# Performance work log

Measured on AMD Instinct MI355X. Metric: run time of the kernel, lower is better.

The kernel has to match this reference:

```python
import jax, jax.numpy as jnp
import numpy as np

N_GROUPS = 4


def setup_inputs() -> dict:
    key = jax.random.key(0)
    ks = jax.random.split(key, 6)
    I, J, B = 512, 512, 4  # query tokens, key tokens, grid batch (B = 1 * n_groups)
    n_dim, out_per_group = 128, 4  # n_heads // n_groups = 16 // 4
    grid_q = jax.random.normal(ks[0], (I, 3), dtype=jnp.float32)
    grid_kv = jax.random.normal(ks[1], (B, J, 3), dtype=jnp.float32)
    W1 = jax.random.normal(ks[2], (3, n_dim), dtype=jnp.float32) * (1.0 / np.sqrt(3))
    b1 = jnp.zeros((n_dim,), dtype=jnp.float32)
    W2 = jax.random.normal(ks[3], (n_dim, n_dim), dtype=jnp.float32) * (1.0 / np.sqrt(n_dim))
    b2 = jnp.zeros((n_dim,), dtype=jnp.float32)
    W3 = jax.random.normal(ks[4], (n_dim, out_per_group), dtype=jnp.float32) * (1.0 / np.sqrt(n_dim))
    b3 = jnp.zeros((out_per_group,), dtype=jnp.float32)
    return {"grid_q": grid_q, "grid_kv": grid_kv, "W1": W1, "b1": b1,
            "W2": W2, "b2": b2, "W3": W3, "b3": b3}


def reference(grid_q, grid_kv, W1, b1, W2, b2, W3, b3):
    # grid_q: [I, 3] -> [1, I, 3]; grid_kv: [B, J, 3]
    gq = grid_q[None, :, :]
    # pairwise position difference: [B, I, J, 3]
    pos = gq[:, :, None, :] - grid_kv[:, None, :, :]
    # sign-log transform
    bias = jnp.sign(pos) * jnp.log1p(jnp.abs(pos))
    # tiny MLP: 3 -> n_dim -> n_dim -> heads//groups, pointwise over (B, I, J)
    h = jax.nn.relu(jnp.einsum('bijc,cd->bijd', bias, W1) + b1)
    h = jax.nn.relu(jnp.einsum('bijd,de->bije', h, W2) + b2)
    out = jnp.einsum('bije,eo->bijo', h, W3) + b3  # [B, I, J, O]
    # rearrange '(b g) i j o -> b (g o) i j' with g = N_GROUPS
    B, I, J, O = out.shape
    out = out.reshape(B // N_GROUPS, N_GROUPS, I, J, O)
    out = jnp.transpose(out, (0, 1, 4, 2, 3)).reshape(B // N_GROUPS, N_GROUPS * O, I, J)
    return out
```

## Files before the change

kernel.cpp:

```cpp
#include <hip/hip_runtime.h>
#include <math.h>

#define NBLOCKS 2048
#define THREADS 512
#define TILE 64
#define POS_PER_BLOCK 512
#define ITERS 8
#define CH 512

typedef __attribute__((ext_vector_type(8)))  short  short8;
typedef __attribute__((ext_vector_type(4)))  float  float4v;
typedef __attribute__((ext_vector_type(4)))  unsigned uint4v;
typedef __attribute__((ext_vector_type(16))) float  float16;

__device__ __forceinline__ unsigned cvt_pk(float lo, float hi) {
    unsigned r;
    asm("v_cvt_pk_bf16_f32 %0, %1, %2" : "=v"(r) : "v"(lo), "v"(hi));
    return r;
}


__device__ __forceinline__ int kmap(int c, int jj) {
    return 32 * (c >> 2) + 16 * ((c >> 1) & 1) + 4 * (c & 1) + ((jj >> 2) << 3) + (jj & 3);
}

__global__ __launch_bounds__(512, 4)
void crpb_mfma8(const float* __restrict__ gq,
                const float* __restrict__ gkv,
                const float* __restrict__ W1,
                const float* __restrict__ b1,
                const float* __restrict__ W2,
                const float* __restrict__ b2,
                const float* __restrict__ W3,
                const float* __restrict__ b3,
                float* __restrict__ out)
{
    __shared__ __align__(16) unsigned short ash[2][16 * CH];
    __shared__ __align__(16) float red[2][4 * 4 * 64];
    __shared__ __align__(16) float b2s[128];
    __shared__ __align__(16) unsigned fA[512][4];
    __shared__ __align__(16) unsigned fB[512];

    const int tid  = threadIdx.x;
    const int lane = tid & 63;
    const int w    = __builtin_amdgcn_readfirstlane(tid >> 6);
    const int l31  = lane & 31;
    const int lh   = lane >> 5;

    if (tid < 128) b2s[tid] = b2[tid];

    const int ct = w & 3;
    const int ph = w >> 2;
    const int pofs = ph * 32 + l31;

    float16 z16;
    #pragma unroll
    for (int r = 0; r < 16; ++r) z16[r] = 0.0f;

    short8 w1f;
    {
        const int ch = ct * 32 + l31;
        const float w0 = W1[ch], w1v = W1[128 + ch], w2v = W1[256 + ch], b1v = b1[ch];
        const float w0h = __uint_as_float(cvt_pk(w0, w0) << 16);
        const float w1h = __uint_as_float(cvt_pk(w1v, w1v) << 16);
        const float w2h = __uint_as_float(cvt_pk(w2v, w2v) << 16);
        const float b1h = __uint_as_float(cvt_pk(b1v, b1v) << 16);
        const float w0l = w0 - w0h, w1l = w1v - w1h, w2l = w2v - w2h, b1l = b1v - b1h;
        unsigned d[4];
        if (lh == 0) {
            d[0] = cvt_pk(w0h, w0l);
            d[1] = cvt_pk(w0h, w1h);
            d[2] = cvt_pk(w1l, w1h);
            d[3] = cvt_pk(w2h, w2l);
        } else {
            d[0] = cvt_pk(w2h, b1h);
            d[1] = cvt_pk(b1l, 0.0f);
            d[2] = 0; d[3] = 0;
        }
        __builtin_memcpy(&w1f, d, 16);
    }

    short8 a2f[8];
    {
        const int e = ct * 32 + l31;
        #pragma unroll
        for (int ks = 0; ks < 8; ++ks) {
            const int c = 2 * ks + lh;
            unsigned t0[4];
            #pragma unroll
            for (int t = 0; t < 4; ++t) {
                const int d0 = kmap(c, 2 * t), d1 = d0 + 1;
                t0[t] = cvt_pk(W2[d0 * 128 + e], W2[d1 * 128 + e]);
            }
            __builtin_memcpy(&a2f[ks], t0, 16);
        }
    }

    short8 w3a[2];
    #pragma unroll
    for (int m2 = 0; m2 < 2; ++m2) {
        unsigned tt[4];
        #pragma unroll
        for (int t = 0; t < 4; ++t) {
            const int chl = ((2 * t) & 3) + 8 * ((2 * t) >> 2) + 4 * lh + 16 * m2;
            const int ch0 = ct * 32 + chl, ch1 = ch0 + 1;
            const float lo = (l31 < 4) ? W3[ch0 * 4 + l31] : 0.0f;
            const float hi = (l31 < 4) ? W3[ch1 * 4 + l31] : 0.0f;
            tt[t] = cvt_pk(lo, hi);
        }
        __builtin_memcpy(&w3a[m2], tt, 16);
    }
    const float b3r = b3[w & 3];

    const int posblock = blockIdx.x * POS_PER_BLOCK;
    const int bb = posblock >> 18;
    const int i  = (posblock >> 9) & 511;
    const float q0 = gq[i * 3 + 0], q1 = gq[i * 3 + 1], q2 = gq[i * 3 + 2];
    const float* kvrow = gkv + (size_t)(bb << 9) * 3;

    for (int jj = tid; jj < 512; jj += THREADS) {
        const float k0 = kvrow[jj * 3 + 0], k1 = kvrow[jj * 3 + 1], k2 = kvrow[jj * 3 + 2];
        const float c0 = q0 - k0, c1 = q1 - k1, c2 = q2 - k2;
        const float f0 = copysignf(__logf(1.0f + fabsf(c0)), c0);
        const float f1 = copysignf(__logf(1.0f + fabsf(c1)), c1);
        const float f2 = copysignf(__logf(1.0f + fabsf(c2)), c2);
        const unsigned u0 = cvt_pk(f0, f0), u2 = cvt_pk(f2, f2);
        const float f0h = __uint_as_float(u0 << 16);
        const float f1h = __uint_as_float(cvt_pk(f1, f1) << 16);
        const float f2h = __uint_as_float(u2 << 16);
        const float f0l = f0 - f0h, f1l = f1 - f1h, f2l = f2 - f2h;
        fA[jj][0] = u0;
        fA[jj][1] = cvt_pk(f0l, f1);
        fA[jj][2] = cvt_pk(f1, f1l);
        fA[jj][3] = u2;
        fB[jj]    = cvt_pk(f2l, 1.0f);
    }
    __syncthreads();

    auto phaseA = [&](int x, int buf) {
        const int jpos = x * TILE + pofs;
        unsigned d[4];
        if (lh == 0) {
            const uint4v t = *(const uint4v*)&fA[jpos][0];
            d[0] = t[0]; d[1] = t[1]; d[2] = t[2]; d[3] = t[3];
        } else {
            d[0] = fB[jpos];
            d[1] = 0x00003F80u;
            d[2] = 0; d[3] = 0;
        }
        short8 bf; __builtin_memcpy(&bf, d, 16);

        float16 c1r = __builtin_amdgcn_mfma_f32_32x32x16_bf16(w1f, bf, z16, 0, 0, 0);
        unsigned pk0[4], pk1[4];
        #pragma unroll
        for (int t = 0; t < 4; ++t) {
            pk0[t] = cvt_pk(fmaxf(c1r[2 * t], 0.f),     fmaxf(c1r[2 * t + 1], 0.f));
            pk1[t] = cvt_pk(fmaxf(c1r[8 + 2 * t], 0.f), fmaxf(c1r[8 + 2 * t + 1], 0.f));
        }
        short8 v0, v1;
        __builtin_memcpy(&v0, pk0, 16);
        __builtin_memcpy(&v1, pk1, 16);
        *(short8*)&ash[buf][(4 * ct + lh) * CH + pofs * 8]     = v0;
        *(short8*)&ash[buf][(4 * ct + 2 + lh) * CH + pofs * 8] = v1;
    };

    phaseA(0, 0);
    __syncthreads();

    for (int it = 0; it < ITERS; ++it) {
        const int buf = it & 1;
        const int jb = it * TILE;

        float16 acc;
        #pragma unroll
        for (int qr = 0; qr < 4; ++qr) {
            float4v i0 = *(const float4v*)&b2s[ct * 32 + 8 * qr + 4 * lh];
            #pragma unroll
            for (int t = 0; t < 4; ++t) acc[4 * qr + t] = i0[t];
        }
        const unsigned short* br = &ash[buf][lh * CH + pofs * 8];

        __builtin_amdgcn_s_setprio(1);
        #pragma unroll
        for (int ks = 0; ks < 8; ++ks) {
            short8 bfrag = *(const short8*)(br + ks * 2 * CH);
            acc = __builtin_amdgcn_mfma_f32_32x32x16_bf16(a2f[ks], bfrag, acc, 0, 0, 0);
        }

        {
            unsigned pa0[4], pa1[4];
            #pragma unroll
            for (int t = 0; t < 4; ++t) {
                pa0[t] = cvt_pk(fmaxf(acc[2 * t], 0.f),     fmaxf(acc[2 * t + 1], 0.f));
                pa1[t] = cvt_pk(fmaxf(acc[8 + 2 * t], 0.f), fmaxf(acc[8 + 2 * t + 1], 0.f));
            }
            short8 fa0, fa1;
            __builtin_memcpy(&fa0, pa0, 16); __builtin_memcpy(&fa1, pa1, 16);
            float16 p;
            p = __builtin_amdgcn_mfma_f32_32x32x16_bf16(w3a[0], fa0, z16, 0, 0, 0);
            p = __builtin_amdgcn_mfma_f32_32x32x16_bf16(w3a[1], fa1, p, 0, 0, 0);
            __builtin_amdgcn_s_setprio(0);
            if (lh == 0) {
                #pragma unroll
                for (int o = 0; o < 4; ++o)
                    red[buf][ct * 256 + o * 64 + pofs] = p[o];
            }
        }

        if (it != ITERS - 1) phaseA(it + 1, 1 - buf);

        __syncthreads();

        if (w < 4) {
            const int o = w, pos = lane;
            const float v = b3r
                          + red[buf][0 * 256 + o * 64 + pos]
                          + red[buf][1 * 256 + o * 64 + pos]
                          + red[buf][2 * 256 + o * 64 + pos]
                          + red[buf][3 * 256 + o * 64 + pos];
            out[((size_t)((bb << 2) + o) << 18) + ((size_t)i << 9) + jb + pos] = v;
        }
    }
}

extern "C" void kernel_launch(void* const* d_in, const int* in_sizes, int n_in,
                              void* d_out, int out_size, void* d_ws, size_t ws_size,
                              hipStream_t stream) {
    const float* gq  = (const float*)d_in[0];
    const float* gkv = (const float*)d_in[1];
    const float* W1  = (const float*)d_in[2];
    const float* b1  = (const float*)d_in[3];
    const float* W2  = (const float*)d_in[4];
    const float* b2  = (const float*)d_in[5];
    const float* W3  = (const float*)d_in[6];
    const float* b3  = (const float*)d_in[7];
    float* out = (float*)d_out;

    crpb_mfma8<<<NBLOCKS, THREADS, 0, stream>>>(gq, gkv, W1, b1, W2, b2, W3, b3, out);
}
```

Before: 118.9 us.

## Halve block size to 256 threads with 32-position tiles and 4096 blocks

Each block now handles half a query row (256 key positions) with 4 waves instead of 8. Each wave covers one 32-channel slice for 32 positions per tile, where before pairs of waves split 64 positions. Shared memory per block is halved, the block count doubles, and the prologue computes features only for the block's own j range. This aims for better occupancy and load balance across CUs, at the cost of twice as many per-block weight-fragment setups and half the MFMA work between barriers.

```diff
diff --git a/kernel.cpp b/kernel.cpp
--- a/kernel.cpp
+++ b/kernel.cpp
@@ -1,12 +1,12 @@
 #include <hip/hip_runtime.h>
 #include <math.h>
 
-#define NBLOCKS 2048
-#define THREADS 512
-#define TILE 64
-#define POS_PER_BLOCK 512
+#define NBLOCKS 4096
+#define THREADS 256
+#define TILE 32
+#define POS_PER_BLOCK 256
 #define ITERS 8
-#define CH 512
+#define CH 256
 
 typedef __attribute__((ext_vector_type(8)))  short  short8;
 typedef __attribute__((ext_vector_type(4)))  float  float4v;
@@ -19,12 +19,11 @@
     return r;
 }
 
-
 __device__ __forceinline__ int kmap(int c, int jj) {
     return 32 * (c >> 2) + 16 * ((c >> 1) & 1) + 4 * (c & 1) + ((jj >> 2) << 3) + (jj & 3);
 }
 
-__global__ __launch_bounds__(512, 4)
+__global__ __launch_bounds__(256, 4)
 void crpb_mfma8(const float* __restrict__ gq,
                 const float* __restrict__ gkv,
                 const float* __restrict__ W1,
@@ -36,10 +35,10 @@
                 float* __restrict__ out)
 {
     __shared__ __align__(16) unsigned short ash[2][16 * CH];
-    __shared__ __align__(16) float red[2][4 * 4 * 64];
+    __shared__ __align__(16) float red[2][4 * 4 * 32];
     __shared__ __align__(16) float b2s[128];
-    __shared__ __align__(16) unsigned fA[512][4];
-    __shared__ __align__(16) unsigned fB[512];
+    __shared__ __align__(16) unsigned fA[256][4];
+    __shared__ __align__(16) unsigned fB[256];
 
     const int tid  = threadIdx.x;
     const int lane = tid & 63;
@@ -49,9 +48,7 @@
 
     if (tid < 128) b2s[tid] = b2[tid];
 
-    const int ct = w & 3;
-    const int ph = w >> 2;
-    const int pofs = ph * 32 + l31;
+    const int ct = w;
 
     float16 z16;
     #pragma unroll
@@ -110,15 +107,17 @@
         }
         __builtin_memcpy(&w3a[m2], tt, 16);
     }
-    const float b3r = b3[w & 3];
+    const float b3r = b3[w];
 
     const int posblock = blockIdx.x * POS_PER_BLOCK;
-    const int bb = posblock >> 18;
-    const int i  = (posblock >> 9) & 511;
+    const int bb    = posblock >> 18;
+    const int i     = (posblock >> 9) & 511;
+    const int jbase = posblock & 511;
     const float q0 = gq[i * 3 + 0], q1 = gq[i * 3 + 1], q2 = gq[i * 3 + 2];
-    const float* kvrow = gkv + (size_t)(bb << 9) * 3;
-
-    for (int jj = tid; jj < 512; jj += THREADS) {
+    const float* kvrow = gkv + (size_t)((bb << 9) + jbase) * 3;
+
+    {
+        const int jj = tid;
         const float k0 = kvrow[jj * 3 + 0], k1 = kvrow[jj * 3 + 1], k2 = kvrow[jj * 3 + 2];
         const float c0 = q0 - k0, c1 = q1 - k1, c2 = q2 - k2;
         const float f0 = copysignf(__logf(1.0f + fabsf(c0)), c0);
@@ -138,13 +137,13 @@
     __syncthreads();
 
     auto phaseA = [&](int x, int buf) {
-        const int jpos = x * TILE + pofs;
+        const int jj = x * TILE + l31;
         unsigned d[4];
         if (lh == 0) {
-            const uint4v t = *(const uint4v*)&fA[jpos][0];
+            const uint4v t = *(const uint4v*)&fA[jj][0];
             d[0] = t[0]; d[1] = t[1]; d[2] = t[2]; d[3] = t[3];
         } else {
-            d[0] = fB[jpos];
+            d[0] = fB[jj];
             d[1] = 0x00003F80u;
             d[2] = 0; d[3] = 0;
         }
@@ -160,8 +159,8 @@
         short8 v0, v1;
         __builtin_memcpy(&v0, pk0, 16);
         __builtin_memcpy(&v1, pk1, 16);
-        *(short8*)&ash[buf][(4 * ct + lh) * CH + pofs * 8]     = v0;
-        *(short8*)&ash[buf][(4 * ct + 2 + lh) * CH + pofs * 8] = v1;
+        *(short8*)&ash[buf][(4 * ct + lh) * CH + l31 * 8]     = v0;
+        *(short8*)&ash[buf][(4 * ct + 2 + lh) * CH + l31 * 8] = v1;
     };
 
     phaseA(0, 0);
@@ -169,7 +168,7 @@
 
     for (int it = 0; it < ITERS; ++it) {
         const int buf = it & 1;
-        const int jb = it * TILE;
+        const int jb = jbase + it * TILE;
 
         float16 acc;
         #pragma unroll
@@ -178,7 +177,7 @@
             #pragma unroll
             for (int t = 0; t < 4; ++t) acc[4 * qr + t] = i0[t];
         }
-        const unsigned short* br = &ash[buf][lh * CH + pofs * 8];
+        const unsigned short* br = &ash[buf][lh * CH + l31 * 8];
 
         __builtin_amdgcn_s_setprio(1);
         #pragma unroll
@@ -203,7 +202,7 @@
             if (lh == 0) {
                 #pragma unroll
                 for (int o = 0; o < 4; ++o)
-                    red[buf][ct * 256 + o * 64 + pofs] = p[o];
+                    red[buf][ct * 128 + o * 32 + l31] = p[o];
             }
         }
 
@@ -211,13 +210,13 @@
 
         __syncthreads();
 
-        if (w < 4) {
-            const int o = w, pos = lane;
+        if (lh == 0) {
+            const int o = w, pos = l31;
             const float v = b3r
-                          + red[buf][0 * 256 + o * 64 + pos]
-                          + red[buf][1 * 256 + o * 64 + pos]
-                          + red[buf][2 * 256 + o * 64 + pos]
-                          + red[buf][3 * 256 + o * 64 + pos];
+                          + red[buf][0 * 128 + o * 32 + pos]
+                          + red[buf][1 * 128 + o * 32 + pos]
+                          + red[buf][2 * 128 + o * 32 + pos]
+                          + red[buf][3 * 128 + o * 32 + pos];
             out[((size_t)((bb << 2) + o) << 18) + ((size_t)i << 9) + jb + pos] = v;
         }
     }
```

Measured after the change: 121.8 us. 2.5% more time.

## Halve block to four waves each processing two position sub-tiles

Applied to the files above, without the earlier changes.

Cuts the block from 8 waves to 4. Each wave now covers both 32-position halves of a 64-position tile with two independent MFMA accumulator chains, so each A-fragment register load of W2 is reused twice. This gives more instruction-level parallelism per wave, and the whole block now does the final reduction and store. The cost is higher register pressure (launch bounds drop to 3 blocks per CU) and fewer waves for latency hiding.

```diff
diff --git a/kernel.cpp b/kernel.cpp
--- a/kernel.cpp
+++ b/kernel.cpp
@@ -2,9 +2,8 @@
 #include <math.h>
 
 #define NBLOCKS 2048
-#define THREADS 512
+#define THREADS 256
 #define TILE 64
-#define POS_PER_BLOCK 512
 #define ITERS 8
 #define CH 512
 
@@ -19,12 +18,11 @@
     return r;
 }
 
-
 __device__ __forceinline__ int kmap(int c, int jj) {
     return 32 * (c >> 2) + 16 * ((c >> 1) & 1) + 4 * (c & 1) + ((jj >> 2) << 3) + (jj & 3);
 }
 
-__global__ __launch_bounds__(512, 4)
+__global__ __launch_bounds__(256, 3)
 void crpb_mfma8(const float* __restrict__ gq,
                 const float* __restrict__ gkv,
                 const float* __restrict__ W1,
@@ -49,9 +47,7 @@
 
     if (tid < 128) b2s[tid] = b2[tid];
 
-    const int ct = w & 3;
-    const int ph = w >> 2;
-    const int pofs = ph * 32 + l31;
+    const int ct = w;
 
     float16 z16;
     #pragma unroll
@@ -110,9 +106,9 @@
         }
         __builtin_memcpy(&w3a[m2], tt, 16);
     }
-    const float b3r = b3[w & 3];
-
-    const int posblock = blockIdx.x * POS_PER_BLOCK;
+    const float b3r = b3[w];
+
+    const int posblock = blockIdx.x * 512;
     const int bb = posblock >> 18;
     const int i  = (posblock >> 9) & 511;
     const float q0 = gq[i * 3 + 0], q1 = gq[i * 3 + 1], q2 = gq[i * 3 + 2];
@@ -138,30 +134,34 @@
     __syncthreads();
 
     auto phaseA = [&](int x, int buf) {
-        const int jpos = x * TILE + pofs;
-        unsigned d[4];
-        if (lh == 0) {
-            const uint4v t = *(const uint4v*)&fA[jpos][0];
-            d[0] = t[0]; d[1] = t[1]; d[2] = t[2]; d[3] = t[3];
-        } else {
-            d[0] = fB[jpos];
-            d[1] = 0x00003F80u;
-            d[2] = 0; d[3] = 0;
-        }
-        short8 bf; __builtin_memcpy(&bf, d, 16);
-
-        float16 c1r = __builtin_amdgcn_mfma_f32_32x32x16_bf16(w1f, bf, z16, 0, 0, 0);
-        unsigned pk0[4], pk1[4];
-        #pragma unroll
-        for (int t = 0; t < 4; ++t) {
-            pk0[t] = cvt_pk(fmaxf(c1r[2 * t], 0.f),     fmaxf(c1r[2 * t + 1], 0.f));
-            pk1[t] = cvt_pk(fmaxf(c1r[8 + 2 * t], 0.f), fmaxf(c1r[8 + 2 * t + 1], 0.f));
-        }
-        short8 v0, v1;
-        __builtin_memcpy(&v0, pk0, 16);
-        __builtin_memcpy(&v1, pk1, 16);
-        *(short8*)&ash[buf][(4 * ct + lh) * CH + pofs * 8]     = v0;
-        *(short8*)&ash[buf][(4 * ct + 2 + lh) * CH + pofs * 8] = v1;
+        #pragma unroll
+        for (int sub = 0; sub < 2; ++sub) {
+            const int pofs = sub * 32 + l31;
+            const int jpos = x * TILE + pofs;
+            unsigned d[4];
+            if (lh == 0) {
+                const uint4v t = *(const uint4v*)&fA[jpos][0];
+                d[0] = t[0]; d[1] = t[1]; d[2] = t[2]; d[3] = t[3];
+            } else {
+                d[0] = fB[jpos];
+                d[1] = 0x00003F80u;
+                d[2] = 0; d[3] = 0;
+            }
+            short8 bf; __builtin_memcpy(&bf, d, 16);
+
+            float16 c1r = __builtin_amdgcn_mfma_f32_32x32x16_bf16(w1f, bf, z16, 0, 0, 0);
+            unsigned pk0[4], pk1[4];
+            #pragma unroll
+            for (int t = 0; t < 4; ++t) {
+                pk0[t] = cvt_pk(fmaxf(c1r[2 * t], 0.f),     fmaxf(c1r[2 * t + 1], 0.f));
+                pk1[t] = cvt_pk(fmaxf(c1r[8 + 2 * t], 0.f), fmaxf(c1r[8 + 2 * t + 1], 0.f));
+            }
+            short8 v0, v1;
+            __builtin_memcpy(&v0, pk0, 16);
+            __builtin_memcpy(&v1, pk1, 16);
+            *(short8*)&ash[buf][(4 * ct + lh) * CH + pofs * 8]     = v0;
+            *(short8*)&ash[buf][(4 * ct + 2 + lh) * CH + pofs * 8] = v1;
+        }
     };
 
     phaseA(0, 0);
@@ -171,23 +171,28 @@
         const int buf = it & 1;
         const int jb = it * TILE;
 
-        float16 acc;
+        float16 acc0, acc1;
         #pragma unroll
         for (int qr = 0; qr < 4; ++qr) {
             float4v i0 = *(const float4v*)&b2s[ct * 32 + 8 * qr + 4 * lh];
             #pragma unroll
-            for (int t = 0; t < 4; ++t) acc[4 * qr + t] = i0[t];
-        }
-        const unsigned short* br = &ash[buf][lh * CH + pofs * 8];
+            for (int t = 0; t < 4; ++t) { acc0[4 * qr + t] = i0[t]; acc1[4 * qr + t] = i0[t]; }
+        }
+        const unsigned short* br0 = &ash[buf][lh * CH + (0 * 32 + l31) * 8];
+        const unsigned short* br1 = &ash[buf][lh * CH + (1 * 32 + l31) * 8];
 
         __builtin_amdgcn_s_setprio(1);
         #pragma unroll
         for (int ks = 0; ks < 8; ++ks) {
-            short8 bfrag = *(const short8*)(br + ks * 2 * CH);
-            acc = __builtin_amdgcn_mfma_f32_32x32x16_bf16(a2f[ks], bfrag, acc, 0, 0, 0);
-        }
-
-        {
+            short8 bf0 = *(const short8*)(br0 + ks * 2 * CH);
+            short8 bf1 = *(const short8*)(br1 + ks * 2 * CH);
+            acc0 = __builtin_amdgcn_mfma_f32_32x32x16_bf16(a2f[ks], bf0, acc0, 0, 0, 0);
+            acc1 = __builtin_amdgcn_mfma_f32_32x32x16_bf16(a2f[ks], bf1, acc1, 0, 0, 0);
+        }
+
+        #pragma unroll
+        for (int sub = 0; sub < 2; ++sub) {
+            const float16& acc = sub ? acc1 : acc0;
             unsigned pa0[4], pa1[4];
             #pragma unroll
             for (int t = 0; t < 4; ++t) {
@@ -199,19 +204,19 @@
             float16 p;
             p = __builtin_amdgcn_mfma_f32_32x32x16_bf16(w3a[0], fa0, z16, 0, 0, 0);
             p = __builtin_amdgcn_mfma_f32_32x32x16_bf16(w3a[1], fa1, p, 0, 0, 0);
-            __builtin_amdgcn_s_setprio(0);
             if (lh == 0) {
                 #pragma unroll
                 for (int o = 0; o < 4; ++o)
-                    red[buf][ct * 256 + o * 64 + pofs] = p[o];
-            }
-        }
+                    red[buf][ct * 256 + o * 64 + sub * 32 + l31] = p[o];
+            }
+        }
+        __builtin_amdgcn_s_setprio(0);
 
         if (it != ITERS - 1) phaseA(it + 1, 1 - buf);
 
         __syncthreads();
 
-        if (w < 4) {
+        {
             const int o = w, pos = lane;
             const float v = b3r
                           + red[buf][0 * 256 + o * 64 + pos]
```

Result: no change. 118.8 us (-0.1%).

## Recompute layer-1 activations in registers per wave instead of sharing via LDS

Applied to the files above, without the earlier changes.

Each wave now computes all 128 first-layer channels for its own positions and feeds them straight into the layer-2 MFMAs from registers. This removes the LDS staging buffers, the prologue feature table and one barrier stage. The b2 bias is injected with an extra MFMA instead of an LDS load. The cost is 4x redundant layer-1 MFMAs and log computations per wave, plus more register pressure from holding four W1 fragments.

```diff
diff --git a/kernel.cpp b/kernel.cpp
--- a/kernel.cpp
+++ b/kernel.cpp
@@ -4,13 +4,10 @@
 #define NBLOCKS 2048
 #define THREADS 512
 #define TILE 64
-#define POS_PER_BLOCK 512
 #define ITERS 8
-#define CH 512
 
 typedef __attribute__((ext_vector_type(8)))  short  short8;
 typedef __attribute__((ext_vector_type(4)))  float  float4v;
-typedef __attribute__((ext_vector_type(4)))  unsigned uint4v;
 typedef __attribute__((ext_vector_type(16))) float  float16;
 
 __device__ __forceinline__ unsigned cvt_pk(float lo, float hi) {
@@ -18,7 +15,6 @@
     asm("v_cvt_pk_bf16_f32 %0, %1, %2" : "=v"(r) : "v"(lo), "v"(hi));
     return r;
 }
-
 
 __device__ __forceinline__ int kmap(int c, int jj) {
     return 32 * (c >> 2) + 16 * ((c >> 1) & 1) + 4 * (c & 1) + ((jj >> 2) << 3) + (jj & 3);
@@ -35,11 +31,7 @@
                 const float* __restrict__ b3,
                 float* __restrict__ out)
 {
-    __shared__ __align__(16) unsigned short ash[2][16 * CH];
-    __shared__ __align__(16) float red[2][4 * 4 * 64];
-    __shared__ __align__(16) float b2s[128];
-    __shared__ __align__(16) unsigned fA[512][4];
-    __shared__ __align__(16) unsigned fB[512];
+    __shared__ float red[2][4][4][64];
 
     const int tid  = threadIdx.x;
     const int lane = tid & 63;
@@ -47,9 +39,7 @@
     const int l31  = lane & 31;
     const int lh   = lane >> 5;
 
-    if (tid < 128) b2s[tid] = b2[tid];
-
-    const int ct = w & 3;
+    const int et = w & 3;
     const int ph = w >> 2;
     const int pofs = ph * 32 + l31;
 
@@ -57,32 +47,33 @@
     #pragma unroll
     for (int r = 0; r < 16; ++r) z16[r] = 0.0f;
 
-    short8 w1f;
-    {
-        const int ch = ct * 32 + l31;
+    short8 w1f[4];
+    #pragma unroll
+    for (int ct4 = 0; ct4 < 4; ++ct4) {
+        const int ch = ct4 * 32 + l31;
         const float w0 = W1[ch], w1v = W1[128 + ch], w2v = W1[256 + ch], b1v = b1[ch];
         const float w0h = __uint_as_float(cvt_pk(w0, w0) << 16);
         const float w1h = __uint_as_float(cvt_pk(w1v, w1v) << 16);
         const float w2h = __uint_as_float(cvt_pk(w2v, w2v) << 16);
         const float b1h = __uint_as_float(cvt_pk(b1v, b1v) << 16);
-        const float w0l = w0 - w0h, w1l = w1v - w1h, w2l = w2v - w2h, b1l = b1v - b1h;
+        const float w0l = w0 - w0h, w1l = w1v - w1h, w2l_ = w2v - w2h, b1l = b1v - b1h;
         unsigned d[4];
         if (lh == 0) {
             d[0] = cvt_pk(w0h, w0l);
             d[1] = cvt_pk(w0h, w1h);
             d[2] = cvt_pk(w1l, w1h);
-            d[3] = cvt_pk(w2h, w2l);
+            d[3] = cvt_pk(w2h, w2l_);
         } else {
             d[0] = cvt_pk(w2h, b1h);
             d[1] = cvt_pk(b1l, 0.0f);
             d[2] = 0; d[3] = 0;
         }
-        __builtin_memcpy(&w1f, d, 16);
+        __builtin_memcpy(&w1f[ct4], d, 16);
     }
 
     short8 a2f[8];
     {
-        const int e = ct * 32 + l31;
+        const int e = et * 32 + l31;
         #pragma unroll
         for (int ks = 0; ks < 8; ++ks) {
             const int c = 2 * ks + lh;
@@ -96,6 +87,20 @@
         }
     }
 
+    short8 b2aA, cstB;
+    {
+        const float b2v = b2[et * 32 + l31];
+        const float b2h = __uint_as_float(cvt_pk(b2v, b2v) << 16);
+        const float b2l = b2v - b2h;
+        unsigned da[4] = {0, 0, 0, 0}, db[4] = {0, 0, 0, 0};
+        if (lh == 0) {
+            da[0] = cvt_pk(b2h, b2l);
+            db[0] = cvt_pk(1.0f, 1.0f);
+        }
+        __builtin_memcpy(&b2aA, da, 16);
+        __builtin_memcpy(&cstB, db, 16);
+    }
+
     short8 w3a[2];
     #pragma unroll
     for (int m2 = 0; m2 < 2; ++m2) {
@@ -103,7 +108,7 @@
         #pragma unroll
         for (int t = 0; t < 4; ++t) {
             const int chl = ((2 * t) & 3) + 8 * ((2 * t) >> 2) + 4 * lh + 16 * m2;
-            const int ch0 = ct * 32 + chl, ch1 = ch0 + 1;
+            const int ch0 = et * 32 + chl, ch1 = ch0 + 1;
             const float lo = (l31 < 4) ? W3[ch0 * 4 + l31] : 0.0f;
             const float hi = (l31 < 4) ? W3[ch1 * 4 + l31] : 0.0f;
             tt[t] = cvt_pk(lo, hi);
@@ -112,15 +117,19 @@
     }
     const float b3r = b3[w & 3];
 
-    const int posblock = blockIdx.x * POS_PER_BLOCK;
+    const int posblock = blockIdx.x * 512;
     const int bb = posblock >> 18;
     const int i  = (posblock >> 9) & 511;
     const float q0 = gq[i * 3 + 0], q1 = gq[i * 3 + 1], q2 = gq[i * 3 + 2];
     const float* kvrow = gkv + (size_t)(bb << 9) * 3;
 
-    for (int jj = tid; jj < 512; jj += THREADS) {
-        const float k0 = kvrow[jj * 3 + 0], k1 = kvrow[jj * 3 + 1], k2 = kvrow[jj * 3 + 2];
-        const float c0 = q0 - k0, c1 = q1 - k1, c2 = q2 - k2;
+
+    for (int it = 0; it < ITERS; ++it) {
+        const int buf = it & 1;
+        const int jpos = it * TILE + pofs;
+
+        const float* kp = kvrow + (size_t)jpos * 3;
+        const float c0 = q0 - kp[0], c1 = q1 - kp[1], c2 = q2 - kp[2];
         const float f0 = copysignf(__logf(1.0f + fabsf(c0)), c0);
         const float f1 = copysignf(__logf(1.0f + fabsf(c1)), c1);
         const float f2 = copysignf(__logf(1.0f + fabsf(c2)), c2);
@@ -129,96 +138,66 @@
         const float f1h = __uint_as_float(cvt_pk(f1, f1) << 16);
         const float f2h = __uint_as_float(u2 << 16);
         const float f0l = f0 - f0h, f1l = f1 - f1h, f2l = f2 - f2h;
-        fA[jj][0] = u0;
-        fA[jj][1] = cvt_pk(f0l, f1);
-        fA[jj][2] = cvt_pk(f1, f1l);
-        fA[jj][3] = u2;
-        fB[jj]    = cvt_pk(f2l, 1.0f);
-    }
-    __syncthreads();
-
-    auto phaseA = [&](int x, int buf) {
-        const int jpos = x * TILE + pofs;
         unsigned d[4];
         if (lh == 0) {
-            const uint4v t = *(const uint4v*)&fA[jpos][0];
-            d[0] = t[0]; d[1] = t[1]; d[2] = t[2]; d[3] = t[3];
+            d[0] = u0;
+            d[1] = cvt_pk(f0l, f1);
+            d[2] = cvt_pk(f1, f1l);
+            d[3] = u2;
         } else {
-            d[0] = fB[jpos];
-            d[1] = 0x00003F80u;
+            d[0] = cvt_pk(f2l, 1.0f);
+            d[1] = cvt_pk(1.0f, 0.0f);
             d[2] = 0; d[3] = 0;
         }
         short8 bf; __builtin_memcpy(&bf, d, 16);
 
-        float16 c1r = __builtin_amdgcn_mfma_f32_32x32x16_bf16(w1f, bf, z16, 0, 0, 0);
-        unsigned pk0[4], pk1[4];
-        #pragma unroll
-        for (int t = 0; t < 4; ++t) {
-            pk0[t] = cvt_pk(fmaxf(c1r[2 * t], 0.f),     fmaxf(c1r[2 * t + 1], 0.f));
-            pk1[t] = cvt_pk(fmaxf(c1r[8 + 2 * t], 0.f), fmaxf(c1r[8 + 2 * t + 1], 0.f));
-        }
-        short8 v0, v1;
-        __builtin_memcpy(&v0, pk0, 16);
-        __builtin_memcpy(&v1, pk1, 16);
-        *(short8*)&ash[buf][(4 * ct + lh) * CH + pofs * 8]     = v0;
-        *(short8*)&ash[buf][(4 * ct + 2 + lh) * CH + pofs * 8] = v1;
-    };
-
-    phaseA(0, 0);
-    __syncthreads();
-
-    for (int it = 0; it < ITERS; ++it) {
-        const int buf = it & 1;
-        const int jb = it * TILE;
-
-        float16 acc;
-        #pragma unroll
-        for (int qr = 0; qr < 4; ++qr) {
-            float4v i0 = *(const float4v*)&b2s[ct * 32 + 8 * qr + 4 * lh];
-            #pragma unroll
-            for (int t = 0; t < 4; ++t) acc[4 * qr + t] = i0[t];
-        }
-        const unsigned short* br = &ash[buf][lh * CH + pofs * 8];
-
         __builtin_amdgcn_s_setprio(1);
-        #pragma unroll
-        for (int ks = 0; ks < 8; ++ks) {
-            short8 bfrag = *(const short8*)(br + ks * 2 * CH);
-            acc = __builtin_amdgcn_mfma_f32_32x32x16_bf16(a2f[ks], bfrag, acc, 0, 0, 0);
-        }
-
-        {
-            unsigned pa0[4], pa1[4];
+        float16 acc = __builtin_amdgcn_mfma_f32_32x32x16_bf16(b2aA, cstB, z16, 0, 0, 0);
+        #pragma unroll
+        for (int ct4 = 0; ct4 < 4; ++ct4) {
+            float16 c1r = __builtin_amdgcn_mfma_f32_32x32x16_bf16(w1f[ct4], bf, z16, 0, 0, 0);
+            unsigned pk0[4], pk1[4];
             #pragma unroll
             for (int t = 0; t < 4; ++t) {
-                pa0[t] = cvt_pk(fmaxf(acc[2 * t], 0.f),     fmaxf(acc[2 * t + 1], 0.f));
-                pa1[t] = cvt_pk(fmaxf(acc[8 + 2 * t], 0.f), fmaxf(acc[8 + 2 * t + 1], 0.f));
+                pk0[t] = cvt_pk(fmaxf(c1r[2 * t], 0.f),     fmaxf(c1r[2 * t + 1], 0.f));
+                pk1[t] = cvt_pk(fmaxf(c1r[8 + 2 * t], 0.f), fmaxf(c1r[8 + 2 * t + 1], 0.f));
             }
-            short8 fa0, fa1;
-            __builtin_memcpy(&fa0, pa0, 16); __builtin_memcpy(&fa1, pa1, 16);
-            float16 p;
-            p = __builtin_amdgcn_mfma_f32_32x32x16_bf16(w3a[0], fa0, z16, 0, 0, 0);
-            p = __builtin_amdgcn_mfma_f32_32x32x16_bf16(w3a[1], fa1, p, 0, 0, 0);
-            __builtin_amdgcn_s_setprio(0);
-            if (lh == 0) {
-                #pragma unroll
-                for (int o = 0; o < 4; ++o)
-                    red[buf][ct * 256 + o * 64 + pofs] = p[o];
-            }
-        }
-
-        if (it != ITERS - 1) phaseA(it + 1, 1 - buf);
+            short8 h0, h1;
+            __builtin_memcpy(&h0, pk0, 16);
+            __builtin_memcpy(&h1, pk1, 16);
+            acc = __builtin_amdgcn_mfma_f32_32x32x16_bf16(a2f[2 * ct4],     h0, acc, 0, 0, 0);
+            acc = __builtin_amdgcn_mfma_f32_32x32x16_bf16(a2f[2 * ct4 + 1], h1, acc, 0, 0, 0);
+        }
+
+        unsigned pa0[4], pa1[4];
+        #pragma unroll
+        for (int t = 0; t < 4; ++t) {
+            pa0[t] = cvt_pk(fmaxf(acc[2 * t], 0.f),     fmaxf(acc[2 * t + 1], 0.f));
+            pa1[t] = cvt_pk(fmaxf(acc[8 + 2 * t], 0.f), fmaxf(acc[8 + 2 * t + 1], 0.f));
+        }
+        short8 fa0, fa1;
+        __builtin_memcpy(&fa0, pa0, 16); __builtin_memcpy(&fa1, pa1, 16);
+        float16 p;
+        p = __builtin_amdgcn_mfma_f32_32x32x16_bf16(w3a[0], fa0, z16, 0, 0, 0);
+        p = __builtin_amdgcn_mfma_f32_32x32x16_bf16(w3a[1], fa1, p, 0, 0, 0);
+        __builtin_amdgcn_s_setprio(0);
+
+        if (lh == 0) {
+            #pragma unroll
+            for (int o = 0; o < 4; ++o)
+                red[buf][et][o][pofs] = p[o];
+        }
 
         __syncthreads();
 
         if (w < 4) {
             const int o = w, pos = lane;
             const float v = b3r
-                          + red[buf][0 * 256 + o * 64 + pos]
-                          + red[buf][1 * 256 + o * 64 + pos]
-                          + red[buf][2 * 256 + o * 64 + pos]
-                          + red[buf][3 * 256 + o * 64 + pos];
-            out[((size_t)((bb << 2) + o) << 18) + ((size_t)i << 9) + jb + pos] = v;
+                          + red[buf][0][o][pos]
+                          + red[buf][1][o][pos]
+                          + red[buf][2][o][pos]
+                          + red[buf][3][o][pos];
+            out[((size_t)((bb << 2) + o) << 18) + ((size_t)i << 9) + it * TILE + pos] = v;
         }
     }
 }
```

Measured after the change: 154.4 us. 29.9% more time.
